# Optimization experiments

Hardware: AMD Instinct MI355X
Metric: run time of the kernel (lower is better)

## Reference

```python
import jax, jax.numpy as jnp
import numpy as np

NUM_HEADS = 32
HEAD_DIM = 128
NUM_KV_HEADS = 8
SCALING = HEAD_DIM ** -0.5


def setup_inputs() -> dict:
    key = jax.random.key(0)
    kq, kk, kv = jax.random.split(key, 3)
    B, S = 2, 2048
    return {
        "query": jax.random.normal(kq, (B, S, NUM_HEADS * HEAD_DIM), dtype=jnp.float32),
        "key": jax.random.normal(kk, (B, S, NUM_KV_HEADS * HEAD_DIM), dtype=jnp.float32),
        "value": jax.random.normal(kv, (B, S, NUM_KV_HEADS * HEAD_DIM), dtype=jnp.float32),
    }


def reference(query, key, value):
    B, S, _ = query.shape
    n_rep = NUM_HEADS // NUM_KV_HEADS
    # [B, H, S, D]
    q = query.reshape(B, S, NUM_HEADS, HEAD_DIM).transpose(0, 2, 1, 3)
    k = key.reshape(B, S, NUM_KV_HEADS, HEAD_DIM).transpose(0, 2, 1, 3)
    v = value.reshape(B, S, NUM_KV_HEADS, HEAD_DIM).transpose(0, 2, 1, 3)
    # repeat_kv: (B, Hkv, S, D) -> (B, Hkv*n_rep, S, D)
    k = jnp.repeat(k, n_rep, axis=1)
    v = jnp.repeat(v, n_rep, axis=1)
    # attention scores [B, H, S, S]
    scores = jnp.einsum("bhqd,bhkd->bhqk", q, k) * SCALING
    causal = jnp.tril(jnp.ones((S, S), dtype=bool))
    scores = jnp.where(causal, scores, -jnp.inf)
    # softmax in fp32, cast back to query dtype
    attn = jax.nn.softmax(scores.astype(jnp.float32), axis=-1).astype(q.dtype)
    out = jnp.einsum("bhqk,bhkd->bhqd", attn, v)
    # back to [B, S, H*D]
    return out.transpose(0, 2, 1, 3).reshape(B, S, NUM_HEADS * HEAD_DIM)
```

## Files before the change

kernel.cpp:

```cpp
#include <hip/hip_runtime.h>

#define B_    2
#define S_    2048
#define H_    32
#define KVH_  8
#define D_    128
#define QB    128
#define KB    64
#define NT_   (S_ / KB)
#define SCALE2 0.12751743f

typedef short  short8 __attribute__((ext_vector_type(8)));
typedef float  f32x4  __attribute__((ext_vector_type(4)));

__device__ inline unsigned short f2bf(float f) {
    unsigned int u = __float_as_uint(f);
    u += 0x7fffu + ((u >> 16) & 1u);
    return (unsigned short)(u >> 16);
}
__device__ __forceinline__ float exp2_fast(float x) {
    float r; asm("v_exp_f32 %0, %1" : "=v"(r) : "v"(x)); return r;
}

__global__ void prep_kernel(const float* __restrict__ k, const float* __restrict__ v,
                            unsigned short* __restrict__ kfb,
                            unsigned short* __restrict__ vfb) {
    __shared__ unsigned short Kt[64][136];
    __shared__ unsigned short Vt[64][132];
    const int t = threadIdx.x;
    const int kt = blockIdx.x, bkvh = blockIdx.y;
    const int b = bkvh >> 3, kvh = bkvh & 7;
    const size_t rs = KVH_ * D_;
    const float* ks = k + ((size_t)(b * S_ + kt * 64)) * rs + kvh * D_;
    const float* vs = v + ((size_t)(b * S_ + kt * 64)) * rs + kvh * D_;
    #pragma unroll
    for (int i = 0; i < 8; ++i) {
        const int row = (t >> 5) + i * 8;
        const int col = (t & 31) * 4;
        const float4 a = *(const float4*)(ks + (size_t)row * rs + col);
        const float4 c = *(const float4*)(vs + (size_t)row * rs + col);
        ushort4 wa, wc;
        wa.x = f2bf(a.x); wa.y = f2bf(a.y); wa.z = f2bf(a.z); wa.w = f2bf(a.w);
        wc.x = f2bf(c.x); wc.y = f2bf(c.y); wc.z = f2bf(c.z); wc.w = f2bf(c.w);
        *(ushort4*)&Kt[row][col] = wa;
        *(ushort4*)&Vt[row][col] = wc;
    }
    __syncthreads();
    const int lane = t & 63, m16 = lane & 15, quad = lane >> 4;
    unsigned short* kout = kfb + (size_t)(bkvh * NT_ + kt) * 16 * 512;
    unsigned short* vout = vfb + (size_t)(bkvh * NT_ + kt) * 16 * 512;
    #pragma unroll
    for (int i = 0; i < 4; ++i) {
        const int g = (t >> 6) * 4 + i;
        const int c = g >> 2, nt = g & 3;
        const short8 kk = *(const short8*)&Kt[nt * 16 + m16][c * 32 + quad * 8];
        *(short8*)(kout + g * 512 + lane * 8) = kk;
        const int c2 = g >> 3, dn = g & 7;
        short8 vv;
        #pragma unroll
        for (int j = 0; j < 8; ++j)
            vv[j] = (short)Vt[c2 * 32 + quad * 8 + j][dn * 16 + m16];
        *(short8*)(vout + g * 512 + lane * 8) = vv;
    }
}

#define KV_TILE_B 16384
#define BUF_B     32768
#define PSH_OFF   65536
#define SMEM_B    (PSH_OFF + 128 * 64 * 2)

__device__ __forceinline__ void gld16(const void* g, void* l) {
    __builtin_amdgcn_global_load_lds(
        (const __attribute__((address_space(1))) unsigned int*)g,
        (__attribute__((address_space(3))) unsigned int*)l, 16, 0, 0);
}

__global__ __launch_bounds__(512, 4) void fa8_kernel(
    const float* __restrict__ q, const unsigned short* __restrict__ kfb,
    const unsigned short* __restrict__ vfb, float* __restrict__ out) {

    __shared__ __align__(16) char smem[SMEM_B];
    unsigned short* Psh = (unsigned short*)(smem + PSH_OFF);

    const int t    = threadIdx.x;
    const int wave = t >> 6;
    const int lane = t & 63;
    const int m16  = lane & 15;
    const int quad = lane >> 4;
    const int hi3  = m16 >> 3;
    const int off3 = m16 & 7;

    const int bh  = blockIdx.y;
    const int b   = bh >> 5;
    const int h   = bh & 31;
    const int kvh = h >> 2;

    const char* kB = (const char*)kfb + (size_t)(b * KVH_ + kvh) * NT_ * KV_TILE_B;
    const char* vB = (const char*)vfb + (size_t)(b * KVH_ + kvh) * NT_ * KV_TILE_B;

    for (int half = 0; half < 2; ++half) {
        const int qtile = half ? (int)blockIdx.x : (S_ / QB - 1 - (int)blockIdx.x);
        const int qbase = qtile * QB;
        const int ktmax = 2 * qtile + 1;

        if (half) __syncthreads();

        #pragma unroll
        for (int r = 0; r < 2; ++r) {
            gld16(kB + r * 8192 + t * 16, smem + r * 8192 + t * 16);
            gld16(vB + r * 8192 + t * 16, smem + KV_TILE_B + r * 8192 + t * 16);
        }

        short8 qf[4];
        {
            const float* qp = q + (size_t)(b * S_ + qbase + wave * 16 + m16) * (H_ * D_) + h * D_;
            #pragma unroll
            for (int c = 0; c < 4; ++c) {
                const float4 x0 = *(const float4*)(qp + c * 32 + quad * 8);
                const float4 x1 = *(const float4*)(qp + c * 32 + quad * 8 + 4);
                short8 f;
                f[0] = (short)f2bf(x0.x); f[1] = (short)f2bf(x0.y);
                f[2] = (short)f2bf(x0.z); f[3] = (short)f2bf(x0.w);
                f[4] = (short)f2bf(x1.x); f[5] = (short)f2bf(x1.y);
                f[6] = (short)f2bf(x1.z); f[7] = (short)f2bf(x1.w);
                qf[c] = f;
            }
        }

        f32x4 o[8];
        #pragma unroll
        for (int i = 0; i < 8; ++i) o[i] = (f32x4){0.f, 0.f, 0.f, 0.f};
        float m_i[4], l_i[4];
        #pragma unroll
        for (int r = 0; r < 4; ++r) { m_i[r] = -INFINITY; l_i[r] = 0.f; }

        __syncthreads();

        for (int ktt = 0; ktt <= ktmax; ++ktt) {
            const int kb  = ktt * KB;
            const int cur = ktt & 1;

            if (ktt < ktmax) {
                char* dst = smem + (cur ^ 1) * BUF_B + t * 16;
                const char* ks = kB + (size_t)(ktt + 1) * KV_TILE_B + t * 16;
                const char* vs = vB + (size_t)(ktt + 1) * KV_TILE_B + t * 16;
                #pragma unroll
                for (int r = 0; r < 2; ++r) {
                    gld16(ks + r * 8192, dst + r * 8192);
                    gld16(vs + r * 8192, dst + KV_TILE_B + r * 8192);
                }
            }
            const unsigned short* Kl = (const unsigned short*)(smem + cur * BUF_B);
            const unsigned short* Vl = Kl + KV_TILE_B / 2;

            f32x4 sa[4];
            #pragma unroll
            for (int nt = 0; nt < 4; ++nt) sa[nt] = (f32x4){0.f, 0.f, 0.f, 0.f};
            #pragma unroll
            for (int c = 0; c < 4; ++c) {
                short8 kf[4];
                #pragma unroll
                for (int nt = 0; nt < 4; ++nt)
                    kf[nt] = *(const short8*)(Kl + (c * 4 + nt) * 512 + lane * 8);
                #pragma unroll
                for (int nt = 0; nt < 4; ++nt)
                    sa[nt] = __builtin_amdgcn_mfma_f32_16x16x32_bf16(qf[c], kf[nt], sa[nt], 0, 0, 0);
            }

            const bool dodiag = (ktt >= 2 * qtile);
            float p[4][4];
            #pragma unroll
            for (int nt = 0; nt < 4; ++nt) {
                #pragma unroll
                for (int r = 0; r < 4; ++r) {
                    float sv = sa[nt][r] * SCALE2;
                    if (dodiag) {
                        const int rowg = qbase + wave * 16 + quad * 4 + r;
                        const int colg = kb + nt * 16 + m16;
                        if (colg > rowg) sv = -INFINITY;
                    }
                    p[nt][r] = sv;
                }
            }
            float mv[4];
            #pragma unroll
            for (int r = 0; r < 4; ++r) {
                float m0 = fmaxf(fmaxf(p[0][r], p[1][r]), fmaxf(p[2][r], p[3][r]));
                m0 = fmaxf(m0, __shfl_xor(m0, 1));
                m0 = fmaxf(m0, __shfl_xor(m0, 2));
                m0 = fmaxf(m0, __shfl_xor(m0, 4));
                m0 = fmaxf(m0, __shfl_xor(m0, 8));
                mv[r] = m0;
            }
            const float dmax = fmaxf(fmaxf(mv[0] - m_i[0], mv[1] - m_i[1]),
                                     fmaxf(mv[2] - m_i[2], mv[3] - m_i[3]));
            if (__any(dmax > 0.f)) {
                #pragma unroll
                for (int r = 0; r < 4; ++r) {
                    const float mnew = fmaxf(m_i[r], mv[r]);
                    const float al = exp2_fast(m_i[r] - mnew);
                    m_i[r] = mnew;
                    l_i[r] *= al;
                    #pragma unroll
                    for (int dn = 0; dn < 8; ++dn) o[dn][r] *= al;
                }
            }
            #pragma unroll
            for (int nt = 0; nt < 4; ++nt) {
                #pragma unroll
                for (int r = 0; r < 4; ++r) {
                    const float e = exp2_fast(p[nt][r] - m_i[r]);
                    l_i[r] += e;
                    const int prow = wave * 16 + quad * 4 + r;
                    const int blk  = (nt * 2 + hi3) ^ (prow & 7);
                    Psh[prow * 64 + blk * 8 + off3] = f2bf(e);
                }
            }
            asm volatile("s_waitcnt lgkmcnt(0)" ::: "memory");
            short8 pf[2];
            {
                const int rrow = wave * 16 + m16;
                pf[0] = *(const short8*)&Psh[rrow * 64 + ((quad ^ off3) << 3)];
                pf[1] = *(const short8*)&Psh[rrow * 64 + (((4 + quad) ^ off3) << 3)];
            }

            #pragma unroll
            for (int dn = 0; dn < 8; ++dn) {
                const short8 vv = *(const short8*)(Vl + dn * 512 + lane * 8);
                o[dn] = __builtin_amdgcn_mfma_f32_16x16x32_bf16(pf[0], vv, o[dn], 0, 0, 0);
            }
            #pragma unroll
            for (int dn = 0; dn < 8; ++dn) {
                const short8 vv = *(const short8*)(Vl + (8 + dn) * 512 + lane * 8);
                o[dn] = __builtin_amdgcn_mfma_f32_16x16x32_bf16(pf[1], vv, o[dn], 0, 0, 0);
            }

            __syncthreads();
        }

        float inv[4];
        #pragma unroll
        for (int r = 0; r < 4; ++r) {
            float rs = l_i[r];
            rs += __shfl_xor(rs, 1);
            rs += __shfl_xor(rs, 2);
            rs += __shfl_xor(rs, 4);
            rs += __shfl_xor(rs, 8);
            inv[r] = 1.f / rs;
        }
        float* Ot = (float*)smem + wave * (16 * 128);
        #pragma unroll
        for (int dn = 0; dn < 8; ++dn)
            #pragma unroll
            for (int r = 0; r < 4; ++r)
                Ot[(quad * 4 + r) * 128 + dn * 16 + m16] = o[dn][r] * inv[r];
        asm volatile("s_waitcnt lgkmcnt(0)" ::: "memory");
        float* og = out + (size_t)(b * S_ + qbase + wave * 16) * (H_ * D_) + h * D_;
        #pragma unroll
        for (int i = 0; i < 8; ++i) {
            const int row = (lane >> 5) + i * 2;
            const int col = (lane & 31) * 4;
            *(float4*)(og + (size_t)row * (H_ * D_) + col) = *(const float4*)(Ot + row * 128 + col);
        }
    }
}

extern "C" void kernel_launch(void* const* d_in, const int* in_sizes, int n_in,
                              void* d_out, int out_size, void* d_ws, size_t ws_size,
                              hipStream_t stream) {
    const float* q = (const float*)d_in[0];
    const float* k = (const float*)d_in[1];
    const float* v = (const float*)d_in[2];
    float* out = (float*)d_out;

    unsigned short* kfb = (unsigned short*)d_ws;
    unsigned short* vfb = (unsigned short*)d_ws + (size_t)B_ * KVH_ * S_ * D_;

    prep_kernel<<<dim3(NT_, B_ * KVH_), dim3(256), 0, stream>>>(k, v, kfb, vfb);
    fa8_kernel<<<dim3(S_ / QB / 2, B_ * H_), dim3(512), 0, stream>>>(q, kfb, vfb, out);
}
```

Baseline: 264.3 us.

## Transpose QK^T MFMA so each lane owns one query row; lazy rescale

Swaps the QK^T MFMA operands so the score tile is transposed and each lane holds a single query row. Row max and sum then reduce within a lane plus two cross-quad shuffles, instead of four shuffles per row. The softmax scale is folded into Q at load time. The online-softmax rescale is skipped unless the max grows by more than a threshold of 8 in log2 units. P is written to LDS as packed bf16 pairs with precomputed addresses. The lazy rescale relies on fp32 headroom to stay accurate, and the output scale factors now need shuffles to map back to the accumulator layout.

```diff
diff --git a/kernel.cpp b/kernel.cpp
--- a/kernel.cpp
+++ b/kernel.cpp
@@ -9,6 +9,7 @@
 #define KB    64
 #define NT_   (S_ / KB)
 #define SCALE2 0.12751743f
+#define THR2  8.0f
 
 typedef short  short8 __attribute__((ext_vector_type(8)));
 typedef float  f32x4  __attribute__((ext_vector_type(4)));
@@ -20,6 +21,11 @@
 }
 __device__ __forceinline__ float exp2_fast(float x) {
     float r; asm("v_exp_f32 %0, %1" : "=v"(r) : "v"(x)); return r;
+}
+__device__ __forceinline__ unsigned int cvt_pk_bf16(float lo, float hi) {
+    unsigned int r;
+    asm("v_cvt_pk_bf16_f32 %0, %1, %2" : "=v"(r) : "v"(lo), "v"(hi));
+    return r;
 }
 
 __global__ void prep_kernel(const float* __restrict__ k, const float* __restrict__ v,
@@ -75,7 +81,7 @@
         (__attribute__((address_space(3))) unsigned int*)l, 16, 0, 0);
 }
 
-__global__ __launch_bounds__(512, 4) void fa8_kernel(
+__global__ __launch_bounds__(512, 4) void fa9_kernel(
     const float* __restrict__ q, const unsigned short* __restrict__ kfb,
     const unsigned short* __restrict__ vfb, float* __restrict__ out) {
 
@@ -87,8 +93,6 @@
     const int lane = t & 63;
     const int m16  = lane & 15;
     const int quad = lane >> 4;
-    const int hi3  = m16 >> 3;
-    const int off3 = m16 & 7;
 
     const int bh  = blockIdx.y;
     const int b   = bh >> 5;
@@ -98,10 +102,19 @@
     const char* kB = (const char*)kfb + (size_t)(b * KVH_ + kvh) * NT_ * KV_TILE_B;
     const char* vB = (const char*)vfb + (size_t)(b * KVH_ + kvh) * NT_ * KV_TILE_B;
 
+    const int prow_base = (wave * 16 + m16) * 64;
+    unsigned short* pw[4];
+    #pragma unroll
+    for (int nt = 0; nt < 4; ++nt)
+        pw[nt] = Psh + prow_base + (((nt * 2 + (quad >> 1)) ^ (m16 & 7)) << 3) + (quad & 1) * 4;
+    const unsigned short* pr0 = Psh + prow_base + (((quad)     ^ (m16 & 7)) << 3);
+    const unsigned short* pr1 = Psh + prow_base + (((4 + quad) ^ (m16 & 7)) << 3);
+
     for (int half = 0; half < 2; ++half) {
         const int qtile = half ? (int)blockIdx.x : (S_ / QB - 1 - (int)blockIdx.x);
         const int qbase = qtile * QB;
         const int ktmax = 2 * qtile + 1;
+        const int qrow  = qbase + wave * 16 + m16;
 
         if (half) __syncthreads();
 
@@ -113,16 +126,16 @@
 
         short8 qf[4];
         {
-            const float* qp = q + (size_t)(b * S_ + qbase + wave * 16 + m16) * (H_ * D_) + h * D_;
+            const float* qp = q + (size_t)(b * S_ + qrow) * (H_ * D_) + h * D_;
             #pragma unroll
             for (int c = 0; c < 4; ++c) {
                 const float4 x0 = *(const float4*)(qp + c * 32 + quad * 8);
                 const float4 x1 = *(const float4*)(qp + c * 32 + quad * 8 + 4);
                 short8 f;
-                f[0] = (short)f2bf(x0.x); f[1] = (short)f2bf(x0.y);
-                f[2] = (short)f2bf(x0.z); f[3] = (short)f2bf(x0.w);
-                f[4] = (short)f2bf(x1.x); f[5] = (short)f2bf(x1.y);
-                f[6] = (short)f2bf(x1.z); f[7] = (short)f2bf(x1.w);
+                f[0] = (short)f2bf(x0.x * SCALE2); f[1] = (short)f2bf(x0.y * SCALE2);
+                f[2] = (short)f2bf(x0.z * SCALE2); f[3] = (short)f2bf(x0.w * SCALE2);
+                f[4] = (short)f2bf(x1.x * SCALE2); f[5] = (short)f2bf(x1.y * SCALE2);
+                f[6] = (short)f2bf(x1.z * SCALE2); f[7] = (short)f2bf(x1.w * SCALE2);
                 qf[c] = f;
             }
         }
@@ -130,9 +143,7 @@
         f32x4 o[8];
         #pragma unroll
         for (int i = 0; i < 8; ++i) o[i] = (f32x4){0.f, 0.f, 0.f, 0.f};
-        float m_i[4], l_i[4];
-        #pragma unroll
-        for (int r = 0; r < 4; ++r) { m_i[r] = -INFINITY; l_i[r] = 0.f; }
+        float m_q = -INFINITY, l_q = 0.f;
 
         __syncthreads();
 
@@ -164,7 +175,7 @@
                     kf[nt] = *(const short8*)(Kl + (c * 4 + nt) * 512 + lane * 8);
                 #pragma unroll
                 for (int nt = 0; nt < 4; ++nt)
-                    sa[nt] = __builtin_amdgcn_mfma_f32_16x16x32_bf16(qf[c], kf[nt], sa[nt], 0, 0, 0);
+                    sa[nt] = __builtin_amdgcn_mfma_f32_16x16x32_bf16(kf[nt], qf[c], sa[nt], 0, 0, 0);
             }
 
             const bool dodiag = (ktt >= 2 * qtile);
@@ -173,56 +184,54 @@
             for (int nt = 0; nt < 4; ++nt) {
                 #pragma unroll
                 for (int r = 0; r < 4; ++r) {
-                    float sv = sa[nt][r] * SCALE2;
+                    float sv = sa[nt][r];
                     if (dodiag) {
-                        const int rowg = qbase + wave * 16 + quad * 4 + r;
-                        const int colg = kb + nt * 16 + m16;
-                        if (colg > rowg) sv = -INFINITY;
+                        const int keyg = kb + nt * 16 + quad * 4 + r;
+                        if (keyg > qrow) sv = -INFINITY;
                     }
                     p[nt][r] = sv;
                 }
             }
-            float mv[4];
-            #pragma unroll
-            for (int r = 0; r < 4; ++r) {
-                float m0 = fmaxf(fmaxf(p[0][r], p[1][r]), fmaxf(p[2][r], p[3][r]));
-                m0 = fmaxf(m0, __shfl_xor(m0, 1));
-                m0 = fmaxf(m0, __shfl_xor(m0, 2));
-                m0 = fmaxf(m0, __shfl_xor(m0, 4));
-                m0 = fmaxf(m0, __shfl_xor(m0, 8));
-                mv[r] = m0;
-            }
-            const float dmax = fmaxf(fmaxf(mv[0] - m_i[0], mv[1] - m_i[1]),
-                                     fmaxf(mv[2] - m_i[2], mv[3] - m_i[3]));
-            if (__any(dmax > 0.f)) {
-                #pragma unroll
-                for (int r = 0; r < 4; ++r) {
-                    const float mnew = fmaxf(m_i[r], mv[r]);
-                    const float al = exp2_fast(m_i[r] - mnew);
-                    m_i[r] = mnew;
-                    l_i[r] *= al;
+            float mv;
+            {
+                float t0 = fmaxf(fmaxf(p[0][0], p[0][1]), fmaxf(p[0][2], p[0][3]));
+                float t1 = fmaxf(fmaxf(p[1][0], p[1][1]), fmaxf(p[1][2], p[1][3]));
+                float t2 = fmaxf(fmaxf(p[2][0], p[2][1]), fmaxf(p[2][2], p[2][3]));
+                float t3 = fmaxf(fmaxf(p[3][0], p[3][1]), fmaxf(p[3][2], p[3][3]));
+                mv = fmaxf(fmaxf(t0, t1), fmaxf(t2, t3));
+                mv = fmaxf(mv, __shfl_xor(mv, 16));
+                mv = fmaxf(mv, __shfl_xor(mv, 32));
+            }
+            if (__any(mv - m_q > THR2)) {
+                const float mnew = fmaxf(m_q, mv);
+                const float al = exp2_fast(m_q - mnew);
+                m_q = mnew;
+                l_q *= al;
+                float alo[4];
+                #pragma unroll
+                for (int r = 0; r < 4; ++r)
+                    alo[r] = __shfl(al, quad * 20 + r);
+                #pragma unroll
+                for (int dn = 0; dn < 8; ++dn)
                     #pragma unroll
-                    for (int dn = 0; dn < 8; ++dn) o[dn][r] *= al;
-                }
+                    for (int r = 0; r < 4; ++r) o[dn][r] *= alo[r];
             }
             #pragma unroll
             for (int nt = 0; nt < 4; ++nt) {
-                #pragma unroll
-                for (int r = 0; r < 4; ++r) {
-                    const float e = exp2_fast(p[nt][r] - m_i[r]);
-                    l_i[r] += e;
-                    const int prow = wave * 16 + quad * 4 + r;
-                    const int blk  = (nt * 2 + hi3) ^ (prow & 7);
-                    Psh[prow * 64 + blk * 8 + off3] = f2bf(e);
-                }
+                const float e0 = exp2_fast(p[nt][0] - m_q);
+                const float e1 = exp2_fast(p[nt][1] - m_q);
+                const float e2 = exp2_fast(p[nt][2] - m_q);
+                const float e3 = exp2_fast(p[nt][3] - m_q);
+                l_q += (e0 + e1) + (e2 + e3);
+                uint2 w;
+                w.x = cvt_pk_bf16(e0, e1);
+                w.y = cvt_pk_bf16(e2, e3);
+                *(uint2*)pw[nt] = w;
             }
             asm volatile("s_waitcnt lgkmcnt(0)" ::: "memory");
             short8 pf[2];
-            {
-                const int rrow = wave * 16 + m16;
-                pf[0] = *(const short8*)&Psh[rrow * 64 + ((quad ^ off3) << 3)];
-                pf[1] = *(const short8*)&Psh[rrow * 64 + (((4 + quad) ^ off3) << 3)];
-            }
+            pf[0] = *(const short8*)pr0;
+            pf[1] = *(const short8*)pr1;
 
             #pragma unroll
             for (int dn = 0; dn < 8; ++dn) {
@@ -238,16 +247,15 @@
             __syncthreads();
         }
 
+        float ls = l_q;
+        ls += __shfl_xor(ls, 16);
+        ls += __shfl_xor(ls, 32);
+        const float inv_q = 1.f / ls;
         float inv[4];
         #pragma unroll
-        for (int r = 0; r < 4; ++r) {
-            float rs = l_i[r];
-            rs += __shfl_xor(rs, 1);
-            rs += __shfl_xor(rs, 2);
-            rs += __shfl_xor(rs, 4);
-            rs += __shfl_xor(rs, 8);
-            inv[r] = 1.f / rs;
-        }
+        for (int r = 0; r < 4; ++r)
+            inv[r] = __shfl(inv_q, quad * 20 + r);
+
         float* Ot = (float*)smem + wave * (16 * 128);
         #pragma unroll
         for (int dn = 0; dn < 8; ++dn)
@@ -277,5 +285,5 @@
     unsigned short* vfb = (unsigned short*)d_ws + (size_t)B_ * KVH_ * S_ * D_;
 
     prep_kernel<<<dim3(NT_, B_ * KVH_), dim3(256), 0, stream>>>(k, v, kfb, vfb);
-    fa8_kernel<<<dim3(S_ / QB / 2, B_ * H_), dim3(512), 0, stream>>>(q, kfb, vfb, out);
-}
+    fa9_kernel<<<dim3(S_ / QB / 2, B_ * H_), dim3(512), 0, stream>>>(q, kfb, vfb, out);
+}
```

Result: faster. 225.9 us (-14.5%).
